# Optimization experiments

Measured on AMD Instinct MI355X. Metric: run time of the kernel, lower is better.

Reference implementation:

```python
import jax, jax.numpy as jnp
import numpy as np

B, NG, FS, D, HH, C = 256, 32, 30, 1024, 3, 1024   # graphs, nodes/graph, feat, embed, heads, per-head dim
EPG = 160                                           # edges per graph
K1, K2, K3 = 26, 13, 4                              # ceil(0.8*32), ceil(0.5*26), ceil(0.3*13)


def gat_conv(x, src, dst, mask, W, a_src, a_dst, bias, N):
    """PyG GATConv (concat heads, negative_slope=0.2, add_self_loops=True), eval mode."""
    loop = jnp.arange(N, dtype=src.dtype)
    s = jnp.concatenate([src, loop])
    d = jnp.concatenate([dst, loop])
    m = jnp.concatenate([mask, jnp.ones((N,), bool)])
    xl = (x @ W).reshape(N, HH, C)                       # [N,H,C]
    al_s = jnp.sum(xl * a_src, -1)                       # [N,H]
    al_d = jnp.sum(xl * a_dst, -1)
    logits = jax.nn.leaky_relu(al_s[s] + al_d[d], negative_slope=0.2)  # [E,H]
    logits = jnp.where(m[:, None], logits, jnp.finfo(x.dtype).min)
    mx = jax.ops.segment_max(logits, d, num_segments=N)  # segment softmax over in-edges
    ex = jnp.where(m[:, None], jnp.exp(logits - mx[d]), 0.0)
    den = jax.ops.segment_sum(ex, d, num_segments=N)
    alpha = ex / den[d]
    out = jax.ops.segment_sum(alpha[:, :, None] * xl[s], d, num_segments=N)  # [N,H,C]
    return out.reshape(N, HH * C) + bias


def topk_pool(x, src, dst, mask, p, n_per, k):
    """PyG TopKPooling: score=tanh((x.p)/||p||); keep top-k per graph; gate kept x by score.
    Uniform graph size n_per -> static k. Dropped edges are masked, not removed."""
    score = jnp.tanh((x @ p) / jnp.linalg.norm(p))           # [B*n_per]
    _, idx = jax.lax.top_k(score.reshape(B, n_per), k)       # [B,k] local indices
    perm = (idx + (jnp.arange(B) * n_per)[:, None]).reshape(-1)
    x_new = x[perm] * score[perm][:, None]                   # [B*k, D]
    new_pos = jnp.full((B * n_per,), -1, jnp.int32).at[perm].set(
        jnp.arange(B * k, dtype=jnp.int32))
    ns, nd = new_pos[src], new_pos[dst]
    m = mask & (ns >= 0) & (nd >= 0)
    return x_new, jnp.where(m, ns, 0), jnp.where(m, nd, 0), m


def setup_inputs() -> dict:
    key = jax.random.key(0)
    ks = jax.random.split(key, 40)
    _n = lambda k, shape, s=0.05: jax.random.normal(k, shape, jnp.float32) * s

    x = jax.random.normal(ks[0], (B * NG, FS), jnp.float32)
    src_l = jax.random.randint(ks[1], (B, EPG), 0, NG)
    dst_l = jax.random.randint(ks[2], (B, EPG), 0, NG)
    offs = (jnp.arange(B) * NG)[:, None]
    edge_index = jnp.stack([(src_l + offs).reshape(-1),
                            (dst_l + offs).reshape(-1)]).astype(jnp.int32)
    batch_index = jnp.repeat(jnp.arange(B), NG).astype(jnp.int32)
    edge_attr = jax.random.normal(ks[3], (B * EPG, 6), jnp.float32)  # unused by model

    d = {"x": x, "edge_attr": edge_attr, "edge_index": edge_index, "batch_index": batch_index}
    ins = [FS, D, D]
    ki = 4
    for i, fin in enumerate(ins, 1):
        d[f"g{i}_W"] = _n(ks[ki], (fin, HH * C)); ki += 1
        d[f"g{i}_as"] = _n(ks[ki], (HH, C)); ki += 1
        d[f"g{i}_ad"] = _n(ks[ki], (HH, C)); ki += 1
        d[f"g{i}_b"] = jnp.zeros((HH * C,), jnp.float32)
        d[f"t{i}_W"] = _n(ks[ki], (HH * C, D)); ki += 1
        d[f"t{i}_b"] = jnp.zeros((D,), jnp.float32)
        d[f"p{i}"] = _n(ks[ki], (D,), 1.0); ki += 1
    d["l1_W"] = _n(ks[ki], (D, 1024)); ki += 1
    d["l1_b"] = jnp.zeros((1024,), jnp.float32)
    d["l2_W"] = _n(ks[ki], (1024, 1)); ki += 1
    d["l2_b"] = jnp.zeros((1,), jnp.float32)
    return d


def reference(x, edge_attr, edge_index, batch_index,
              g1_W, g1_as, g1_ad, g1_b, t1_W, t1_b, p1,
              g2_W, g2_as, g2_ad, g2_b, t2_W, t2_b, p2,
              g3_W, g3_as, g3_ad, g3_b, t3_W, t3_b, p3,
              l1_W, l1_b, l2_W, l2_b):
    src, dst = edge_index[0], edge_index[1]
    mask = jnp.ones(src.shape, bool)

    h = gat_conv(x, src, dst, mask, g1_W, g1_as, g1_ad, g1_b, B * NG)
    h = h @ t1_W + t1_b
    h, src, dst, mask = topk_pool(h, src, dst, mask, p1, NG, K1)
    x1 = h.reshape(B, K1, D).mean(1)                     # gap

    h = gat_conv(h, src, dst, mask, g2_W, g2_as, g2_ad, g2_b, B * K1)
    h = h @ t2_W + t2_b
    h, src, dst, mask = topk_pool(h, src, dst, mask, p2, K1, K2)
    x2 = h.reshape(B, K2, D).mean(1)

    h = gat_conv(h, src, dst, mask, g3_W, g3_as, g3_ad, g3_b, B * K2)
    h = h @ t3_W + t3_b
    h, src, dst, mask = topk_pool(h, src, dst, mask, p3, K2, K3)
    x3 = h.reshape(B, K3, D).mean(1)

    z = x1 + x2 + x3
    z = jax.nn.relu(z @ l1_W + l1_b)                     # dropout off (eval)
    return z @ l2_W + l2_b                               # [B, 1]
```

## Files before the change

### kernel.cpp

```cpp
#include <hip/hip_runtime.h>
#include <cstdint>
#include <cstddef>

#define EPG 160
#define HC  3072
#define DD  1024

typedef _Float16 f16x8 __attribute__((ext_vector_type(8)));
typedef _Float16 f16x2 __attribute__((ext_vector_type(2)));
typedef float    f32x4 __attribute__((ext_vector_type(4)));

__device__ __forceinline__ unsigned fenc(float f){
  unsigned u = __float_as_uint(f);
  return (u & 0x80000000u) ? ~u : (u | 0x80000000u);
}
__device__ __forceinline__ float fdec(unsigned u){
  return (u & 0x80000000u) ? __uint_as_float(u ^ 0x80000000u) : __uint_as_float(~u);
}

__device__ __forceinline__ void gload16(const void* g, void* l) {
  __builtin_amdgcn_global_load_lds((const __attribute__((address_space(1))) void*)g,
                                   (__attribute__((address_space(3))) void*)l, 16, 0, 0);
}

__global__ __launch_bounds__(256) void wtrans_kernel(
    const float* __restrict__ W, _Float16* __restrict__ WTh, _Float16* __restrict__ WTl,
    int K, int Nn)
{
  __shared__ float t[32][33];
  const int tx = threadIdx.x, ty = threadIdx.y;
  const int n0 = blockIdx.x * 32, k0 = blockIdx.y * 32;
  #pragma unroll
  for (int i = 0; i < 4; i++) {
    int k = k0 + ty + i * 8;
    t[ty + i * 8][tx] = (k < K) ? W[(size_t)k * Nn + n0 + tx] : 0.f;
  }
  __syncthreads();
  const int kt = k0 >> 5;
  const int c  = tx >> 3;
  const int w8 = tx & 7;
  #pragma unroll
  for (int i = 0; i < 4; i++) {
    int n = n0 + ty + i * 8;
    float v = t[tx][ty + i * 8];
    _Float16 h = (_Float16)v;
    float r = v - (float)h;
    int c2 = c ^ ((n >> 1) & 3);
    size_t addr = ((size_t)kt * Nn + n) * 32 + c2 * 8 + w8;
    WTh[addr] = h;
    WTl[addr] = (_Float16)r;
  }
}

__global__ __launch_bounds__(256) void xsplit_kernel(
    const float* __restrict__ x, _Float16* __restrict__ ATh, _Float16* __restrict__ ATl, int M)
{
  int r = blockIdx.x * 256 + threadIdx.x;
  if (r >= M) return;
  const float* xr = x + (size_t)r * 30;
  float v[32];
  #pragma unroll
  for (int j = 0; j < 32; j++) v[j] = (j < 30) ? xr[j] : 0.f;
  const int sz = (r >> 1) & 3;
  #pragma unroll
  for (int ch = 0; ch < 4; ch++) {
    int c2 = ch ^ sz;
    f16x8 hh, ll;
    #pragma unroll
    for (int j = 0; j < 8; j++) {
      float vv = v[ch * 8 + j];
      _Float16 hv = (_Float16)vv;
      hh[j] = hv; ll[j] = (_Float16)(vv - (float)hv);
    }
    *(f16x8*)&ATh[(size_t)r * 32 + c2 * 8] = hh;
    *(f16x8*)&ATl[(size_t)r * 32 + c2 * 8] = ll;
  }
}

__global__ __launch_bounds__(256) void mfma_gemm(
    const _Float16* __restrict__ ATh, const _Float16* __restrict__ ATl,
    const _Float16* __restrict__ BTh, const _Float16* __restrict__ BTl,
    const float* __restrict__ bias, float* __restrict__ C,
    int M, int N, int K,
    const float* __restrict__ avs, const float* __restrict__ avd,
    float* __restrict__ alsp, float* __restrict__ aldp,
    const float* __restrict__ pvec, float* __restrict__ scp)
{
  __shared__ __align__(16) char smem[2 * 32768];

  const int gx = N >> 7, gy = M >> 7;
  const int lid = blockIdx.x + gx * blockIdx.y;
  int vx, vy;
  const int G = gy & ~7;
  if (lid < gx * G) {
    const int sub = lid & 7, rest = lid >> 3;
    vx = rest % gx; vy = (rest / gx) * 8 + sub;
  } else {
    const int r = lid - gx * G;
    vx = r % gx; vy = G + r / gx;
  }
  const int brow = vy << 7, bcol = vx << 7;

  const int tid  = threadIdx.x;
  const int lane = tid & 63;
  const int w    = tid >> 6;
  const int wr   = (w >> 1) << 6, wc = (w & 1) << 6;
  const int wn   = w & 1;
  const int fr   = lane & 15, g4 = lane >> 4;

  f32x4 acc[4][4];
  #pragma unroll
  for (int m = 0; m < 4; m++)
    #pragma unroll
    for (int n = 0; n < 4; n++) acc[m][n] = (f32x4)0.0f;

  int aoff[4], boff[4];
  #pragma unroll
  for (int m = 0; m < 4; m++) {
    int r = wr + m * 16 + fr;
    aoff[m] = r * 64 + ((g4 ^ ((r >> 1) & 3)) << 4);
  }
  #pragma unroll
  for (int n = 0; n < 4; n++) {
    int r = wc + n * 16 + fr;
    boff[n] = r * 64 + ((g4 ^ ((r >> 1) & 3)) << 4);
  }

  const int ktiles = (K + 31) >> 5;

#define STAGE(ktv, buf)                                                    \
  do {                                                                     \
    char* bse = (buf);                                                     \
    const size_t ab = ((size_t)(ktv) * M + brow) << 6;                     \
    const size_t bb = ((size_t)(ktv) * N + bcol) << 6;                     \
    const char* gah = (const char*)ATh + ab + tid * 16;                    \
    const char* gal = (const char*)ATl + ab + tid * 16;                    \
    const char* gbh = (const char*)BTh + bb + tid * 16;                    \
    const char* gbl = (const char*)BTl + bb + tid * 16;                    \
    gload16(gah,        bse + tid * 16);                                   \
    gload16(gah + 4096, bse + tid * 16 + 4096);                            \
    gload16(gal,        bse + 8192 + tid * 16);                            \
    gload16(gal + 4096, bse + 8192 + tid * 16 + 4096);                     \
    gload16(gbh,        bse + 16384 + tid * 16);                           \
    gload16(gbh + 4096, bse + 16384 + tid * 16 + 4096);                    \
    gload16(gbl,        bse + 24576 + tid * 16);                           \
    gload16(gbl + 4096, bse + 24576 + tid * 16 + 4096);                    \
  } while (0)

  STAGE(0, smem);
  if (ktiles > 1) STAGE(1, smem + 32768);

  for (int kt = 0; kt < ktiles; kt++) {
    char* curb = smem + ((kt & 1) << 15);
    if (kt + 1 < ktiles) {
      asm volatile("s_waitcnt vmcnt(8)" ::: "memory");
    } else {
      asm volatile("s_waitcnt vmcnt(0)" ::: "memory");
    }
    __builtin_amdgcn_s_barrier();
    asm volatile("" ::: "memory");

    f16x8 ah[4], al[4], bh[4], bl[4];
    #pragma unroll
    for (int n = 0; n < 4; n++) {
      bh[n] = *(const f16x8*)(curb + 16384 + boff[n]);
      bl[n] = *(const f16x8*)(curb + 24576 + boff[n]);
    }
    #pragma unroll
    for (int m = 0; m < 4; m++) {
      ah[m] = *(const f16x8*)(curb + aoff[m]);
      al[m] = *(const f16x8*)(curb + 8192 + aoff[m]);
    }
    asm volatile("s_waitcnt lgkmcnt(0)" ::: "memory");
    __builtin_amdgcn_sched_barrier(0);
    __builtin_amdgcn_s_barrier();
    asm volatile("" ::: "memory");

    if (kt + 2 < ktiles) STAGE(kt + 2, curb);

    __builtin_amdgcn_s_setprio(1);
    #pragma unroll
    for (int m = 0; m < 4; m++) {
      #pragma unroll
      for (int n = 0; n < 4; n++) {
        acc[m][n] = __builtin_amdgcn_mfma_f32_16x16x32_f16(ah[m], bh[n], acc[m][n], 0, 0, 0);
        acc[m][n] = __builtin_amdgcn_mfma_f32_16x16x32_f16(al[m], bh[n], acc[m][n], 0, 0, 0);
        acc[m][n] = __builtin_amdgcn_mfma_f32_16x16x32_f16(ah[m], bl[n], acc[m][n], 0, 0, 0);
      }
    }
    __builtin_amdgcn_s_setprio(0);
    asm volatile("" ::: "memory");
  }
#undef STAGE

  const int crow0 = brow + wr + g4 * 4;
  const int ccol0 = bcol + wc + fr;
  #pragma unroll
  for (int n = 0; n < 4; n++) {
    const int col = ccol0 + n * 16;
    const float bv = bias ? bias[col] : 0.f;
    #pragma unroll
    for (int m = 0; m < 4; m++) {
      const int row = crow0 + m * 16;
      #pragma unroll
      for (int q = 0; q < 4; q++)
        C[(size_t)(row + q) * N + col] = acc[m][n][q] + bv;
    }
  }

  if (alsp) {
    const int h3 = bcol >> 10;
    const int slot = ((bcol & 1023) >> 6) + wn;
    #pragma unroll
    for (int m = 0; m < 4; m++) {
      #pragma unroll
      for (int q = 0; q < 4; q++) {
        float ps = 0.f, pd = 0.f;
        #pragma unroll
        for (int n = 0; n < 4; n++) {
          const int col = ccol0 + n * 16;
          const float v = acc[m][n][q];
          ps += v * avs[col]; pd += v * avd[col];
        }
        #pragma unroll
        for (int mk = 1; mk <= 8; mk <<= 1) {
          ps += __shfl_xor(ps, mk);
          pd += __shfl_xor(pd, mk);
        }
        if (fr == 0) {
          const int row = crow0 + m * 16 + q;
          alsp[row * 48 + h3 * 16 + slot] = ps;
          aldp[row * 48 + h3 * 16 + slot] = pd;
        }
      }
    }
  }
  if (scp) {
    const int slot = (bcol >> 6) + wn;
    #pragma unroll
    for (int m = 0; m < 4; m++) {
      #pragma unroll
      for (int q = 0; q < 4; q++) {
        float pp = 0.f;
        #pragma unroll
        for (int n = 0; n < 4; n++) {
          const int col = ccol0 + n * 16;
          pp += (acc[m][n][q] + bias[col]) * pvec[col];
        }
        #pragma unroll
        for (int mk = 1; mk <= 8; mk <<= 1) pp += __shfl_xor(pp, mk);
        if (fr == 0) scp[(crow0 + m * 16 + q) * 16 + slot] = pp;
      }
    }
  }
}

__global__ __launch_bounds__(256) void norm_kernel(
    const float* __restrict__ p1, const float* __restrict__ p2,
    const float* __restrict__ p3, float* __restrict__ nrm)
{
  const float* p = blockIdx.x == 0 ? p1 : (blockIdx.x == 1 ? p2 : p3);
  __shared__ float red[4];
  int tid = threadIdx.x;
  float s = 0.f;
  for (int i = tid; i < DD; i += 256) { float v = p[i]; s += v * v; }
  #pragma unroll
  for (int off = 32; off; off >>= 1) s += __shfl_down(s, off);
  if ((tid & 63) == 0) red[tid >> 6] = s;
  __syncthreads();
  if (tid == 0) nrm[blockIdx.x] = sqrtf(red[0] + red[1] + red[2] + red[3]);
}

__global__ __launch_bounds__(256) void gat_agg(
    const float* __restrict__ xl, const float* __restrict__ alsp, const float* __restrict__ aldp,
    const int* __restrict__ esrc, const int* __restrict__ edst, const int* __restrict__ emask,
    const float* __restrict__ gbias, _Float16* __restrict__ ATh, _Float16* __restrict__ ATl,
    int npg, int Mtot)
{
  const int g = blockIdx.x;
  const int h = blockIdx.y >> 1;
  const int half = blockIdx.y & 1;
  const int tid = threadIdx.x;
  const int base = g * npg;
  __shared__ float sxl[32 * 512];
  __shared__ float s_as[32], s_ad[32], s_mx[32], s_den[32], s_self[32];
  __shared__ unsigned s_mxu[32];
  __shared__ float s_alpha[EPG];
  __shared__ int s_srcl[EPG];
  __shared__ int s_start[33];
  __shared__ int s_cnt[32], s_cur[32];
  __shared__ int s_list[EPG];

  const int colb = h * DD + (half << 9);
  for (int n = 0; n < npg; n++) {
    *(float2*)&sxl[(n << 9) + (tid << 1)] =
        *(const float2*)&xl[(size_t)(base + n) * HC + colb + (tid << 1)];
  }

  if (tid < npg) {
    const float* ps = alsp + (size_t)(base + tid) * 48 + h * 16;
    const float* pdp = aldp + (size_t)(base + tid) * 48 + h * 16;
    float ss = 0.f, dd2 = 0.f;
    #pragma unroll
    for (int s = 0; s < 16; s++) { ss += ps[s]; dd2 += pdp[s]; }
    s_as[tid] = ss;
    s_ad[tid] = dd2;
    s_mxu[tid] = 0u;
    s_den[tid] = 0.f;
    s_cnt[tid] = 0;
    s_cur[tid] = 0;
  }
  __syncthreads();

  int ok = 0, dl = 0;
  float lg = 0.f;
  if (tid < EPG) {
    int ei = g * EPG + tid;
    ok = emask ? emask[ei] : 1;
    if (ok) {
      int sl = esrc[ei] - base;
      dl = edst[ei] - base;
      s_srcl[tid] = sl;
      float v = s_as[sl] + s_ad[dl];
      lg = v > 0.f ? v : 0.2f * v;
      atomicMax(&s_mxu[dl], fenc(lg));
      atomicAdd(&s_cnt[dl], 1);
    }
  }
  float slg = 0.f;
  if (tid < npg) {
    float v = s_as[tid] + s_ad[tid];
    slg = v > 0.f ? v : 0.2f * v;
    atomicMax(&s_mxu[tid], fenc(slg));
  }
  __syncthreads();

  if (tid < npg) s_mx[tid] = fdec(s_mxu[tid]);
  if (tid == 0) {
    int run = 0;
    for (int n = 0; n < npg; n++) { s_start[n] = run; run += s_cnt[n]; }
    s_start[npg] = run;
  }
  __syncthreads();

  float ex = 0.f;
  if (tid < EPG && ok) {
    ex = expf(lg - s_mx[dl]);
    atomicAdd(&s_den[dl], ex);
    int p = s_start[dl] + atomicAdd(&s_cur[dl], 1);
    s_list[p] = tid;
  }
  if (tid < npg) {
    float e2 = expf(slg - s_mx[tid]);
    s_self[tid] = e2;
    atomicAdd(&s_den[tid], e2);
  }
  __syncthreads();

  if (tid < EPG && ok) s_alpha[tid] = ex / s_den[dl];
  if (tid < npg) s_self[tid] = s_self[tid] / s_den[tid];
  __syncthreads();

  const int c = colb + (tid << 1);
  const float b0 = gbias[c], b1 = gbias[c + 1];
  const int kt = c >> 5;
  const int ch = (c >> 3) & 3;
  const int j2 = c & 7;
  for (int n = 0; n < npg; n++) {
    const float2 v = *(const float2*)&sxl[(n << 9) + (tid << 1)];
    float a0 = s_self[n];
    float ax = a0 * v.x, ay = a0 * v.y;
    const int st = s_start[n], en = s_start[n + 1];
    for (int q = st; q < en; q++) {
      int e = s_list[q];
      float a = s_alpha[e];
      const float2 u = *(const float2*)&sxl[(s_srcl[e] << 9) + (tid << 1)];
      ax += a * u.x; ay += a * u.y;
    }
    ax += b0; ay += b1;
    const int R = base + n;
    const int c2 = ch ^ ((R >> 1) & 3);
    const size_t ad = ((size_t)kt * Mtot + R) * 32 + c2 * 8 + j2;
    f16x2 hh, ll;
    _Float16 h0 = (_Float16)ax; hh[0] = h0; ll[0] = (_Float16)(ax - (float)h0);
    _Float16 h1 = (_Float16)ay; hh[1] = h1; ll[1] = (_Float16)(ay - (float)h1);
    *(f16x2*)&ATh[ad] = hh;
    *(f16x2*)&ATl[ad] = ll;
  }
}

__global__ __launch_bounds__(256) void pool_kernel(
    const float* __restrict__ hbuf, const float* __restrict__ scp,
    const int* __restrict__ cs, const int* __restrict__ cd, const int* __restrict__ cm,
    int npg, int k, int Mnext,
    _Float16* __restrict__ ATh, _Float16* __restrict__ ATl,
    float* __restrict__ gap,
    int* __restrict__ ns, int* __restrict__ nd, int* __restrict__ nm,
    const float* __restrict__ nrm, int stage)
{
  int g = blockIdx.x, tid = threadIdx.x;
  __shared__ float ssc[32];
  __shared__ int sord[32];
  __shared__ int snp[32];
  __shared__ float sgp[2][1024];
  if (tid < npg) {
    const float* sp = scp + (size_t)(g * npg + tid) * 16;
    float s = 0.f;
    #pragma unroll
    for (int q = 0; q < 16; q++) s += sp[q];
    ssc[tid] = tanhf(s / nrm[stage]);
  }
  __syncthreads();
  if (tid == 0) {
    for (int i = 0; i < npg; i++) sord[i] = i;
    for (int i = 1; i < npg; i++) {
      int oi = sord[i]; float v = ssc[oi]; int j = i - 1;
      while (j >= 0 && ssc[sord[j]] < v) { sord[j + 1] = sord[j]; j--; }
      sord[j + 1] = oi;
    }
  }
  __syncthreads();
  if (tid < npg) snp[tid] = -1;
  __syncthreads();
  if (tid < k) snp[sord[tid]] = tid;
  __syncthreads();

  const int col0 = (tid & 127) << 3;
  const int rr = tid >> 7;
  const int kt = col0 >> 5;
  const int ch = (col0 >> 3) & 3;
  float part[8];
  #pragma unroll
  for (int j = 0; j < 8; j++) part[j] = 0.f;
  for (int r = rr; r < k; r += 2) {
    int ol = sord[r];
    float s = ssc[ol];
    const float* hr = hbuf + (size_t)(g * npg + ol) * DD + col0;
    float4 v0 = *(const float4*)hr;
    float4 v1 = *(const float4*)(hr + 4);
    float gv[8] = {v0.x * s, v0.y * s, v0.z * s, v0.w * s,
                   v1.x * s, v1.y * s, v1.z * s, v1.w * s};
    #pragma unroll
    for (int j = 0; j < 8; j++) part[j] += gv[j];
    if (ATh) {
      int R = g * k + r;
      int c2 = ch ^ ((R >> 1) & 3);
      size_t ad = ((size_t)kt * Mnext + R) * 32 + c2 * 8;
      f16x8 hh, ll;
      #pragma unroll
      for (int j = 0; j < 8; j++) {
        _Float16 hv = (_Float16)gv[j];
        hh[j] = hv; ll[j] = (_Float16)(gv[j] - (float)hv);
      }
      *(f16x8*)&ATh[ad] = hh;
      *(f16x8*)&ATl[ad] = ll;
    }
  }
  #pragma unroll
  for (int j = 0; j < 8; j++) sgp[rr][col0 + j] = part[j];
  __syncthreads();
  const float fk = (float)k;
  #pragma unroll
  for (int j = 0; j < 4; j++) {
    int cc = tid * 4 + j;
    gap[(size_t)g * DD + cc] = (sgp[0][cc] + sgp[1][cc]) / fk;
  }

  for (int e = tid; e < EPG; e += 256) {
    int ei = g * EPG + e;
    int ok = cm ? cm[ei] : 1;
    int m2 = 0, a = 0, b2 = 0;
    if (ok) {
      int sl = cs[ei] - g * npg, dl = cd[ei] - g * npg;
      int nsl = snp[sl], ndl = snp[dl];
      if (nsl >= 0 && ndl >= 0) { m2 = 1; a = g * k + nsl; b2 = g * k + ndl; }
    }
    ns[ei] = a; nd[ei] = b2; nm[ei] = m2;
  }
}

__global__ __launch_bounds__(256) void head_kernel(
    const float* __restrict__ X1, const float* __restrict__ X2, const float* __restrict__ X3,
    const float* __restrict__ l1W, const float* __restrict__ l1b,
    const float* __restrict__ l2W, float* __restrict__ partial)
{
  __shared__ float a[4][1024];
  __shared__ float red[4][4];
  const int tid = threadIdx.x;
  const int cg = blockIdx.x, rg = blockIdx.y;
  const int row0 = rg << 2;
  #pragma unroll
  for (int r = 0; r < 4; r++) {
    const size_t ro = (size_t)(row0 + r) << 10;
    #pragma unroll
    for (int jj = 0; jj < 4; jj++) {
      int j = tid + jj * 256;
      a[r][j] = X1[ro + j] + X2[ro + j] + X3[ro + j];
    }
  }
  __syncthreads();

  const int col = (cg << 8) + tid;
  float acc0 = 0.f, acc1 = 0.f, acc2 = 0.f, acc3 = 0.f;
  #pragma unroll 8
  for (int k = 0; k < 1024; k++) {
    float wv = l1W[((size_t)k << 10) + col];
    acc0 += a[0][k] * wv;
    acc1 += a[1][k] * wv;
    acc2 += a[2][k] * wv;
    acc3 += a[3][k] * wv;
  }
  const float bv = l1b[col], lw = l2W[col];
  float v0 = fmaxf(acc0 + bv, 0.f) * lw;
  float v1 = fmaxf(acc1 + bv, 0.f) * lw;
  float v2 = fmaxf(acc2 + bv, 0.f) * lw;
  float v3 = fmaxf(acc3 + bv, 0.f) * lw;
  #pragma unroll
  for (int off = 32; off; off >>= 1) {
    v0 += __shfl_down(v0, off);
    v1 += __shfl_down(v1, off);
    v2 += __shfl_down(v2, off);
    v3 += __shfl_down(v3, off);
  }
  const int lane = tid & 63, wid = tid >> 6;
  if (lane == 0) { red[wid][0] = v0; red[wid][1] = v1; red[wid][2] = v2; red[wid][3] = v3; }
  __syncthreads();
  if (tid < 4)
    partial[(size_t)(row0 + tid) * 4 + cg] =
        red[0][tid] + red[1][tid] + red[2][tid] + red[3][tid];
}

__global__ __launch_bounds__(256) void head2_kernel(
    const float* __restrict__ partial, const float* __restrict__ l2b,
    float* __restrict__ out)
{
  int r = threadIdx.x;
  out[r] = partial[r * 4 + 0] + partial[r * 4 + 1] +
           partial[r * 4 + 2] + partial[r * 4 + 3] + l2b[0];
}

extern "C" void kernel_launch(void* const* d_in, const int* in_sizes, int n_in,
                              void* d_out, int out_size, void* d_ws, size_t ws_size,
                              hipStream_t stream)
{
  (void)in_sizes; (void)n_in; (void)out_size; (void)ws_size;
  const float* x    = (const float*)d_in[0];
  const int*   eidx = (const int*)d_in[2];
  const float* g1W = (const float*)d_in[4];
  const float* g1as= (const float*)d_in[5];
  const float* g1ad= (const float*)d_in[6];
  const float* g1b = (const float*)d_in[7];
  const float* t1W = (const float*)d_in[8];
  const float* t1b = (const float*)d_in[9];
  const float* p1  = (const float*)d_in[10];
  const float* g2W = (const float*)d_in[11];
  const float* g2as= (const float*)d_in[12];
  const float* g2ad= (const float*)d_in[13];
  const float* g2b = (const float*)d_in[14];
  const float* t2W = (const float*)d_in[15];
  const float* t2b = (const float*)d_in[16];
  const float* p2  = (const float*)d_in[17];
  const float* g3W = (const float*)d_in[18];
  const float* g3as= (const float*)d_in[19];
  const float* g3ad= (const float*)d_in[20];
  const float* g3b = (const float*)d_in[21];
  const float* t3W = (const float*)d_in[22];
  const float* t3b = (const float*)d_in[23];
  const float* p3  = (const float*)d_in[24];
  const float* l1W = (const float*)d_in[25];
  const float* l1b = (const float*)d_in[26];
  const float* l2W = (const float*)d_in[27];
  const float* l2b = (const float*)d_in[28];
  float* outp = (float*)d_out;

  float* W = (float*)d_ws;
  size_t o = 0;
  float* bufA = W + o; o += (size_t)8192 * HC;
  float* bufB = W + o; o += (size_t)8192 * DD;
  _Float16* ATh = (_Float16*)(W + o); o += (size_t)96 * 8192 * 32 / 2;
  _Float16* ATl = (_Float16*)(W + o); o += (size_t)96 * 8192 * 32 / 2;
  float* ALSp = W + o; o += 8192 * 48;
  float* ALDp = W + o; o += 8192 * 48;
  float* SCp  = W + o; o += 8192 * 16;
  float* NRM = W + o; o += 4;
  float* X1  = W + o; o += 256 * DD;
  float* X2  = W + o; o += 256 * DD;
  float* X3  = W + o; o += 256 * DD;
  float* HP  = W + o; o += 256 * 4;
  int* E0s = (int*)(W + o); o += 40960;
  int* E0d = (int*)(W + o); o += 40960;
  int* E0m = (int*)(W + o); o += 40960;
  int* E1s = (int*)(W + o); o += 40960;
  int* E1d = (int*)(W + o); o += 40960;
  int* E1m = (int*)(W + o); o += 40960;
  _Float16* WTH = (_Float16*)(W + o); o += (3200 * 1024) / 2;
  _Float16* WTL = (_Float16*)(W + o); o += (3200 * 1024) / 2;

  const int* es1 = eidx;
  const int* ed1 = eidx + 40960;

  norm_kernel<<<3, 256, 0, stream>>>(p1, p2, p3, NRM);

  xsplit_kernel<<<32, 256, 0, stream>>>(x, ATh, ATl, 8192);
  wtrans_kernel<<<dim3(96, 1), dim3(32, 8), 0, stream>>>(g1W, WTH, WTL, 30, HC);
  mfma_gemm<<<dim3(24, 64), 256, 0, stream>>>(ATh, ATl, WTH, WTL, nullptr, bufA, 8192, HC, 30,
                                              g1as, g1ad, ALSp, ALDp, nullptr, nullptr);
  gat_agg<<<dim3(256, 6), 256, 0, stream>>>(bufA, ALSp, ALDp, es1, ed1, nullptr, g1b,
                                            ATh, ATl, 32, 8192);
  wtrans_kernel<<<dim3(32, 96), dim3(32, 8), 0, stream>>>(t1W, WTH, WTL, HC, DD);
  mfma_gemm<<<dim3(8, 64), 256, 0, stream>>>(ATh, ATl, WTH, WTL, t1b, bufB, 8192, DD, HC,
                                             nullptr, nullptr, nullptr, nullptr, p1, SCp);
  pool_kernel<<<256, 256, 0, stream>>>(bufB, SCp, es1, ed1, nullptr, 32, 26, 6656,
                                       ATh, ATl, X1, E0s, E0d, E0m, NRM, 0);

  wtrans_kernel<<<dim3(96, 32), dim3(32, 8), 0, stream>>>(g2W, WTH, WTL, DD, HC);
  mfma_gemm<<<dim3(24, 52), 256, 0, stream>>>(ATh, ATl, WTH, WTL, nullptr, bufA, 6656, HC, DD,
                                              g2as, g2ad, ALSp, ALDp, nullptr, nullptr);
  gat_agg<<<dim3(256, 6), 256, 0, stream>>>(bufA, ALSp, ALDp, E0s, E0d, E0m, g2b,
                                            ATh, ATl, 26, 6656);
  wtrans_kernel<<<dim3(32, 96), dim3(32, 8), 0, stream>>>(t2W, WTH, WTL, HC, DD);
  mfma_gemm<<<dim3(8, 52), 256, 0, stream>>>(ATh, ATl, WTH, WTL, t2b, bufB, 6656, DD, HC,
                                             nullptr, nullptr, nullptr, nullptr, p2, SCp);
  pool_kernel<<<256, 256, 0, stream>>>(bufB, SCp, E0s, E0d, E0m, 26, 13, 3328,
                                       ATh, ATl, X2, E1s, E1d, E1m, NRM, 1);

  wtrans_kernel<<<dim3(96, 32), dim3(32, 8), 0, stream>>>(g3W, WTH, WTL, DD, HC);
  mfma_gemm<<<dim3(24, 26), 256, 0, stream>>>(ATh, ATl, WTH, WTL, nullptr, bufA, 3328, HC, DD,
                                              g3as, g3ad, ALSp, ALDp, nullptr, nullptr);
  gat_agg<<<dim3(256, 6), 256, 0, stream>>>(bufA, ALSp, ALDp, E1s, E1d, E1m, g3b,
                                            ATh, ATl, 13, 3328);
  wtrans_kernel<<<dim3(32, 96), dim3(32, 8), 0, stream>>>(t3W, WTH, WTL, HC, DD);
  mfma_gemm<<<dim3(8, 26), 256, 0, stream>>>(ATh, ATl, WTH, WTL, t3b, bufB, 3328, DD, HC,
                                             nullptr, nullptr, nullptr, nullptr, p3, SCp);
  pool_kernel<<<256, 256, 0, stream>>>(bufB, SCp, E1s, E1d, E1m, 13, 4, 1024,
                                       nullptr, nullptr, X3, E0s, E0d, E0m, NRM, 2);

  head_kernel<<<dim3(4, 64), 256, 0, stream>>>(X1, X2, X3, l1W, l1b, l2W, HP);
  head2_kernel<<<1, 256, 0, stream>>>(HP, l2b, outp);
}
```

Before: 954.1 us.

## Fuse first GAT layer projection, attention and aggregation into one kernel

Replaces the xsplit, weight-transpose, split-fp16 MFMA GEMM and gat_agg sequence for layer 1 with a single kernel. Each block computes its graph's 32x30 by 30x1024 projection in fp32 registers, builds a dense 32x32 attention matrix in shared memory and multiplies it in directly. The attention logits come from weights pre-contracted with the attention vectors (W·a) in a new prep kernel, which also absorbs the norm computation. This removes the large 8192x3072 intermediate round-trip through global memory and several launches, at the cost of redoing the projection with scalar FMAs and high register pressure (64 accumulators plus 60 weights per thread).

```diff
diff --git a/kernel.cpp b/kernel.cpp
--- a/kernel.cpp
+++ b/kernel.cpp
@@ -52,28 +52,148 @@
   }
 }
 
-__global__ __launch_bounds__(256) void xsplit_kernel(
-    const float* __restrict__ x, _Float16* __restrict__ ATh, _Float16* __restrict__ ATl, int M)
-{
-  int r = blockIdx.x * 256 + threadIdx.x;
-  if (r >= M) return;
-  const float* xr = x + (size_t)r * 30;
-  float v[32];
-  #pragma unroll
-  for (int j = 0; j < 32; j++) v[j] = (j < 30) ? xr[j] : 0.f;
-  const int sz = (r >> 1) & 3;
-  #pragma unroll
-  for (int ch = 0; ch < 4; ch++) {
-    int c2 = ch ^ sz;
-    f16x8 hh, ll;
-    #pragma unroll
-    for (int j = 0; j < 8; j++) {
-      float vv = v[ch * 8 + j];
-      _Float16 hv = (_Float16)vv;
-      hh[j] = hv; ll[j] = (_Float16)(vv - (float)hv);
-    }
-    *(f16x8*)&ATh[(size_t)r * 32 + c2 * 8] = hh;
-    *(f16x8*)&ATl[(size_t)r * 32 + c2 * 8] = ll;
+__global__ __launch_bounds__(256) void prep_kernel(
+    const float* __restrict__ p1, const float* __restrict__ p2, const float* __restrict__ p3,
+    const float* __restrict__ g1W, const float* __restrict__ g1as, const float* __restrict__ g1ad,
+    float* __restrict__ nrm, float* __restrict__ was, float* __restrict__ wad)
+{
+  const int b = blockIdx.x;
+  const int tid = threadIdx.x;
+  __shared__ float red[4];
+  if (b < 3) {
+    const float* p = b == 0 ? p1 : (b == 1 ? p2 : p3);
+    float s = 0.f;
+    for (int i = tid; i < DD; i += 256) { float v = p[i]; s += v * v; }
+    #pragma unroll
+    for (int off = 32; off; off >>= 1) s += __shfl_down(s, off);
+    if ((tid & 63) == 0) red[tid >> 6] = s;
+    __syncthreads();
+    if (tid == 0) nrm[b] = sqrtf(red[0] + red[1] + red[2] + red[3]);
+  } else {
+    const int idx = b - 3;
+    const int h = idx >> 1;
+    const float* av = (idx & 1) ? g1ad : g1as;
+    float* outv = (idx & 1) ? wad : was;
+    for (int j = 0; j < 30; j++) {
+      float s = 0.f;
+      for (int c = tid; c < DD; c += 256)
+        s += g1W[(size_t)j * HC + h * DD + c] * av[h * DD + c];
+      #pragma unroll
+      for (int off = 32; off; off >>= 1) s += __shfl_down(s, off);
+      if ((tid & 63) == 0) red[tid >> 6] = s;
+      __syncthreads();
+      if (tid == 0) outv[h * 32 + j] = red[0] + red[1] + red[2] + red[3];
+      __syncthreads();
+    }
+    if (tid == 0) { outv[h * 32 + 30] = 0.f; outv[h * 32 + 31] = 0.f; }
+  }
+}
+
+__global__ __launch_bounds__(256) void gat_fused1(
+    const float* __restrict__ x, const float* __restrict__ g1W,
+    const float* __restrict__ was, const float* __restrict__ wad,
+    const int* __restrict__ esrc, const int* __restrict__ edst,
+    const float* __restrict__ gbias,
+    _Float16* __restrict__ ATh, _Float16* __restrict__ ATl, int Mtot)
+{
+  const int g = blockIdx.x;
+  const int h = blockIdx.y >> 1;
+  const int half = blockIdx.y & 1;
+  const int tid = threadIdx.x;
+  const int base = g << 5;
+  __shared__ float sx[32][32];
+  __shared__ float sP[32][33];
+  __shared__ float s_as[32], s_ad[32], s_mx[32], s_den[32];
+  __shared__ unsigned s_mxu[32];
+
+  for (int i = tid; i < 1024; i += 256) {
+    int n = i >> 5, j = i & 31;
+    sx[n][j] = (j < 30) ? x[(size_t)(base + n) * 30 + j] : 0.f;
+  }
+  for (int i = tid; i < 32 * 33; i += 256) ((float*)sP)[i] = 0.f;
+  if (tid < 32) { s_mxu[tid] = 0u; s_den[tid] = 0.f; }
+  __syncthreads();
+
+  const int colb = h * DD + (half << 9);
+  const int c = colb + (tid << 1);
+  float w0[30], w1[30];
+  #pragma unroll
+  for (int j = 0; j < 30; j++) {
+    float2 wv = *(const float2*)&g1W[(size_t)j * HC + c];
+    w0[j] = wv.x; w1[j] = wv.y;
+  }
+
+  if (tid < 32) {
+    float ps = 0.f, pd2 = 0.f;
+    #pragma unroll
+    for (int j = 0; j < 30; j++) {
+      float xv = sx[tid][j];
+      ps  += xv * was[h * 32 + j];
+      pd2 += xv * wad[h * 32 + j];
+    }
+    s_as[tid] = ps; s_ad[tid] = pd2;
+  }
+  __syncthreads();
+
+  int sl = 0, dl = 0;
+  float lg = 0.f;
+  if (tid < EPG) {
+    int ei = g * EPG + tid;
+    sl = esrc[ei] - base; dl = edst[ei] - base;
+    float v = s_as[sl] + s_ad[dl];
+    lg = v > 0.f ? v : 0.2f * v;
+    atomicMax(&s_mxu[dl], fenc(lg));
+  }
+  float slg = 0.f;
+  if (tid < 32) {
+    float v = s_as[tid] + s_ad[tid];
+    slg = v > 0.f ? v : 0.2f * v;
+    atomicMax(&s_mxu[tid], fenc(slg));
+  }
+  __syncthreads();
+  if (tid < 32) s_mx[tid] = fdec(s_mxu[tid]);
+  __syncthreads();
+  float ex = 0.f;
+  if (tid < EPG) { ex = expf(lg - s_mx[dl]); atomicAdd(&s_den[dl], ex); }
+  float exs = 0.f;
+  if (tid < 32) { exs = expf(slg - s_mx[tid]); atomicAdd(&s_den[tid], exs); }
+  __syncthreads();
+  if (tid < EPG) atomicAdd(&sP[dl][sl], ex / s_den[dl]);
+  if (tid < 32)  atomicAdd(&sP[tid][tid], exs / s_den[tid]);
+
+  float xl0[32], xl1[32];
+  #pragma unroll
+  for (int n = 0; n < 32; n++) {
+    float a0 = 0.f, a1 = 0.f;
+    #pragma unroll
+    for (int j = 0; j < 30; j++) {
+      float xv = sx[n][j];
+      a0 += xv * w0[j]; a1 += xv * w1[j];
+    }
+    xl0[n] = a0; xl1[n] = a1;
+  }
+  __syncthreads();
+
+  const float b0 = gbias[c], b1 = gbias[c + 1];
+  const int kt = c >> 5;
+  const int ch = (c >> 3) & 3;
+  const int j2 = c & 7;
+  for (int n = 0; n < 32; n++) {
+    float a0 = 0.f, a1 = 0.f;
+    #pragma unroll
+    for (int m = 0; m < 32; m++) {
+      float p = sP[n][m];
+      a0 += p * xl0[m]; a1 += p * xl1[m];
+    }
+    a0 += b0; a1 += b1;
+    const int R = base + n;
+    const int c2 = ch ^ ((R >> 1) & 3);
+    const size_t ad = ((size_t)kt * Mtot + R) * 32 + c2 * 8 + j2;
+    f16x2 hh, ll;
+    _Float16 h0 = (_Float16)a0; hh[0] = h0; ll[0] = (_Float16)(a0 - (float)h0);
+    _Float16 h1 = (_Float16)a1; hh[1] = h1; ll[1] = (_Float16)(a1 - (float)h1);
+    *(f16x2*)&ATh[ad] = hh;
+    *(f16x2*)&ATl[ad] = ll;
   }
 }
 
@@ -253,22 +373,6 @@
       }
     }
   }
-}
-
-__global__ __launch_bounds__(256) void norm_kernel(
-    const float* __restrict__ p1, const float* __restrict__ p2,
-    const float* __restrict__ p3, float* __restrict__ nrm)
-{
-  const float* p = blockIdx.x == 0 ? p1 : (blockIdx.x == 1 ? p2 : p3);
-  __shared__ float red[4];
-  int tid = threadIdx.x;
-  float s = 0.f;
-  for (int i = tid; i < DD; i += 256) { float v = p[i]; s += v * v; }
-  #pragma unroll
-  for (int off = 32; off; off >>= 1) s += __shfl_down(s, off);
-  if ((tid & 63) == 0) red[tid >> 6] = s;
-  __syncthreads();
-  if (tid == 0) nrm[blockIdx.x] = sqrtf(red[0] + red[1] + red[2] + red[3]);
 }
 
 __global__ __launch_bounds__(256) void gat_agg(
@@ -583,6 +687,8 @@
   float* ALDp = W + o; o += 8192 * 48;
   float* SCp  = W + o; o += 8192 * 16;
   float* NRM = W + o; o += 4;
+  float* WAS = W + o; o += 96;
+  float* WAD = W + o; o += 96;
   float* X1  = W + o; o += 256 * DD;
   float* X2  = W + o; o += 256 * DD;
   float* X3  = W + o; o += 256 * DD;
@@ -599,14 +705,9 @@
   const int* es1 = eidx;
   const int* ed1 = eidx + 40960;
 
-  norm_kernel<<<3, 256, 0, stream>>>(p1, p2, p3, NRM);
-
-  xsplit_kernel<<<32, 256, 0, stream>>>(x, ATh, ATl, 8192);
-  wtrans_kernel<<<dim3(96, 1), dim3(32, 8), 0, stream>>>(g1W, WTH, WTL, 30, HC);
-  mfma_gemm<<<dim3(24, 64), 256, 0, stream>>>(ATh, ATl, WTH, WTL, nullptr, bufA, 8192, HC, 30,
-                                              g1as, g1ad, ALSp, ALDp, nullptr, nullptr);
-  gat_agg<<<dim3(256, 6), 256, 0, stream>>>(bufA, ALSp, ALDp, es1, ed1, nullptr, g1b,
-                                            ATh, ATl, 32, 8192);
+  prep_kernel<<<9, 256, 0, stream>>>(p1, p2, p3, g1W, g1as, g1ad, NRM, WAS, WAD);
+  gat_fused1<<<dim3(256, 6), 256, 0, stream>>>(x, g1W, WAS, WAD, es1, ed1, g1b,
+                                               ATh, ATl, 8192);
   wtrans_kernel<<<dim3(32, 96), dim3(32, 8), 0, stream>>>(t1W, WTH, WTL, HC, DD);
   mfma_gemm<<<dim3(8, 64), 256, 0, stream>>>(ATh, ATl, WTH, WTL, t1b, bufB, 8192, DD, HC,
                                              nullptr, nullptr, nullptr, nullptr, p1, SCp);
```

Result: no change. 946.8 us (-0.8%).
